# Performance work log

Measured on AMD Instinct MI355X. Metric: run time of the kernel, lower is better.

## Reference

```python
import jax, jax.numpy as jnp
import numpy as np

B, S, E, H, D = 4, 2048, 1024, 16, 64

def setup_inputs() -> dict:
    key = jax.random.key(0)
    ks = jax.random.split(key, 9)
    sc = 0.02
    return {
        "x":  jax.random.normal(ks[0], (B, S, E), jnp.float32),
        "Wq": jax.random.normal(ks[1], (H, E, D), jnp.float32) * sc,
        "bq": jax.random.normal(ks[2], (H, D), jnp.float32) * sc,
        "Wk": jax.random.normal(ks[3], (H, E, D), jnp.float32) * sc,
        "bk": jax.random.normal(ks[4], (H, D), jnp.float32) * sc,
        "Wv": jax.random.normal(ks[5], (H, E, D), jnp.float32) * sc,
        "bv": jax.random.normal(ks[6], (H, D), jnp.float32) * sc,
        "Wp": jax.random.normal(ks[7], (H * D, E), jnp.float32) * sc,
        "bp": jax.random.normal(ks[8], (E,), jnp.float32) * sc,
    }

def reference(x, Wq, bq, Wk, bk, Wv, bv, Wp, bp):
    # Per-head projections (stacked): [B,S,E] x [H,E,D] -> [B,H,S,D]
    q = jnp.einsum('bse,hed->bhsd', x, Wq) + bq[None, :, None, :]
    k = jnp.einsum('bse,hed->bhsd', x, Wk) + bk[None, :, None, :]
    v = jnp.einsum('bse,hed->bhsd', x, Wv) + bv[None, :, None, :]
    # Scaled scores with causal mask: [B,H,S,S]
    scores = jnp.einsum('bhqd,bhkd->bhqk', q, k) / jnp.sqrt(jnp.float32(D))
    causal = jnp.tril(jnp.ones((S, S), dtype=bool))
    scores = jnp.where(causal[None, None], scores, -jnp.inf)
    attn = jax.nn.softmax(scores, axis=-1)
    out = jnp.einsum('bhqk,bhkd->bhqd', attn, v)          # [B,H,S,D]
    out = out.transpose(0, 2, 1, 3).reshape(B, S, H * D)  # concat heads
    return out @ Wp + bp                                   # [B,S,E]
```

## Files before the change

kernel.cpp:

```cpp
#include <hip/hip_runtime.h>
#include <hip/hip_bf16.h>

#define B_ 4
#define S_ 2048
#define E_ 1024
#define H_ 16
#define D_ 64
#define QSCALE 0.18033688011112042f

typedef __attribute__((ext_vector_type(8))) short bf16x8;
typedef __attribute__((ext_vector_type(4))) float f32x4;
typedef __attribute__((ext_vector_type(16))) float f32x16;

__device__ __forceinline__ f32x4 mfma16(bf16x8 a, bf16x8 b, f32x4 c) {
    return __builtin_amdgcn_mfma_f32_16x16x32_bf16(a, b, c, 0, 0, 0);
}
__device__ __forceinline__ f32x16 mfma32(bf16x8 a, bf16x8 b, f32x16 c) {
    return __builtin_amdgcn_mfma_f32_32x32x16_bf16(a, b, c, 0, 0, 0);
}
__device__ __forceinline__ short f2bs(float f) {
    __hip_bfloat16 h = __float2bfloat16(f);
    return *reinterpret_cast<short*>(&h);
}

#define XSLAB 1032
#define WSLAB 1544

__global__ __launch_bounds__(256) void conv_wqkv(
    const float* __restrict__ Wq, const float* __restrict__ Wk,
    const float* __restrict__ Wv, short* __restrict__ WT)
{
    const int mat = blockIdx.x >> 4;
    const int kt  = blockIdx.x & 15;
    const int which = mat >> 4, h = mat & 15;
    const float* src = (which == 0 ? Wq : which == 1 ? Wk : Wv) + (size_t)h * E_ * D_;
    __shared__ float T[64][65];
    const int tid = threadIdx.x;
    const int k0 = kt * 64;
    #pragma unroll
    for (int it = 0; it < 4; ++it) {
        int lin = tid + it * 256;
        int kr = lin >> 4, dc = (lin & 15) * 4;
        const float4 v = *(const float4*)&src[(size_t)(k0 + kr) * D_ + dc];
        T[kr][dc] = v.x; T[kr][dc + 1] = v.y; T[kr][dc + 2] = v.z; T[kr][dc + 3] = v.w;
    }
    __syncthreads();
    #pragma unroll
    for (int it = 0; it < 4; ++it) {
        int lin = tid + it * 256;
        int dr = lin >> 4, kc = (lin & 15) * 4;
        ushort4 o;
        o.x = (unsigned short)f2bs(T[kc][dr]);
        o.y = (unsigned short)f2bs(T[kc + 1][dr]);
        o.z = (unsigned short)f2bs(T[kc + 2][dr]);
        o.w = (unsigned short)f2bs(T[kc + 3][dr]);
        *(ushort4*)&WT[((size_t)mat * 64 + dr) * E_ + k0 + kc] = o;
    }
}

__global__ __launch_bounds__(256) void conv_wp(
    const float* __restrict__ Wp, short* __restrict__ WpT)
{
    const int ktile = blockIdx.x & 15, ntile = blockIdx.x >> 4;
    const int k0 = ktile * 64, n0 = ntile * 64;
    __shared__ float T[64][65];
    const int tid = threadIdx.x;
    #pragma unroll
    for (int it = 0; it < 4; ++it) {
        int lin = tid + it * 256;
        int kr = lin >> 4, nc = (lin & 15) * 4;
        const float4 v = *(const float4*)&Wp[(size_t)(k0 + kr) * E_ + n0 + nc];
        T[kr][nc] = v.x; T[kr][nc + 1] = v.y; T[kr][nc + 2] = v.z; T[kr][nc + 3] = v.w;
    }
    __syncthreads();
    #pragma unroll
    for (int it = 0; it < 4; ++it) {
        int lin = tid + it * 256;
        int nr = lin >> 4, kc = (lin & 15) * 4;
        ushort4 o;
        o.x = (unsigned short)f2bs(T[kc][nr]);
        o.y = (unsigned short)f2bs(T[kc + 1][nr]);
        o.z = (unsigned short)f2bs(T[kc + 2][nr]);
        o.w = (unsigned short)f2bs(T[kc + 3][nr]);
        *(ushort4*)&WpT[(size_t)(n0 + nr) * E_ + k0 + kc] = o;
    }
}

__global__ __launch_bounds__(256, 2) void qkv_fused(
    const float* __restrict__ x, const short* __restrict__ WT,
    const float* __restrict__ bq, const float* __restrict__ bk,
    const float* __restrict__ bv,
    short* __restrict__ Qw, short* __restrict__ Kw, short* __restrict__ VTw)
{
    const int h = blockIdx.y;
    const int m0 = blockIdx.x * 128;
    __shared__ short SM[8 * XSLAB + 8 * WSLAB];
    short* Xs = SM;
    short* Ws = SM + 8 * XSLAB;

    const int tid = threadIdx.x;
    const int lane = tid & 63, w = tid >> 6;
    const int wm = w & 1, wn = w >> 1;
    const int l31 = lane & 31, hi = lane >> 5;
    const int cc = tid & 7, r8 = tid >> 3;

    f32x16 acc[2][3];
    #pragma unroll
    for (int mf = 0; mf < 2; ++mf)
        #pragma unroll
        for (int nf = 0; nf < 3; ++nf)
            #pragma unroll
            for (int i = 0; i < 16; ++i) acc[mf][nf][i] = 0.f;

    float4 xr[4][2];
    bf16x8 wr[6];

    #pragma unroll
    for (int it = 0; it < 4; ++it) {
        const float* p = &x[(size_t)(m0 + it * 32 + r8) * E_ + cc * 8];
        xr[it][0] = *(const float4*)p;
        xr[it][1] = *(const float4*)(p + 4);
    }
    #pragma unroll
    for (int it = 0; it < 6; ++it) {
        int rg = ((it >> 1) * 16 + h) * 64 + (it & 1) * 32 + r8;
        wr[it] = *(const bf16x8*)&WT[(size_t)rg * E_ + cc * 8];
    }

    for (int k0 = 0; k0 < E_; k0 += 64) {
        #pragma unroll
        for (int it = 0; it < 4; ++it) {
            bf16x8 pk;
            pk[0] = f2bs(xr[it][0].x); pk[1] = f2bs(xr[it][0].y);
            pk[2] = f2bs(xr[it][0].z); pk[3] = f2bs(xr[it][0].w);
            pk[4] = f2bs(xr[it][1].x); pk[5] = f2bs(xr[it][1].y);
            pk[6] = f2bs(xr[it][1].z); pk[7] = f2bs(xr[it][1].w);
            *(bf16x8*)&Xs[cc * XSLAB + (it * 32 + r8) * 8] = pk;
        }
        #pragma unroll
        for (int it = 0; it < 6; ++it)
            *(bf16x8*)&Ws[cc * WSLAB + (it * 32 + r8) * 8] = wr[it];
        __syncthreads();
        if (k0 + 64 < E_) {
            #pragma unroll
            for (int it = 0; it < 4; ++it) {
                const float* p = &x[(size_t)(m0 + it * 32 + r8) * E_ + k0 + 64 + cc * 8];
                xr[it][0] = *(const float4*)p;
                xr[it][1] = *(const float4*)(p + 4);
            }
            #pragma unroll
            for (int it = 0; it < 6; ++it) {
                int rg = ((it >> 1) * 16 + h) * 64 + (it & 1) * 32 + r8;
                wr[it] = *(const bf16x8*)&WT[(size_t)rg * E_ + k0 + 64 + cc * 8];
            }
        }
        #pragma unroll
        for (int ks = 0; ks < 4; ++ks) {
            const int ccr = ks * 2 + hi;
            bf16x8 a[2], b[3];
            #pragma unroll
            for (int mf = 0; mf < 2; ++mf)
                a[mf] = *(const bf16x8*)&Xs[ccr * XSLAB + (wm * 64 + mf * 32 + l31) * 8];
            #pragma unroll
            for (int nf = 0; nf < 3; ++nf)
                b[nf] = *(const bf16x8*)&Ws[ccr * WSLAB + (wn * 96 + nf * 32 + l31) * 8];
            #pragma unroll
            for (int mf = 0; mf < 2; ++mf)
                #pragma unroll
                for (int nf = 0; nf < 3; ++nf)
                    acc[mf][nf] = mfma32(a[mf], b[nf], acc[mf][nf]);
        }
        __syncthreads();
    }

    const int bb = m0 >> 11;
    const int s0 = m0 & (S_ - 1);
    const size_t qkbase = ((size_t)bb * H_ + h) * S_;
    short* Vr = SM;
    #pragma unroll
    for (int mf = 0; mf < 2; ++mf)
        #pragma unroll
        for (int nf = 0; nf < 3; ++nf) {
            const int ng = wn * 96 + nf * 32;
            const int mat = ng >> 6;
            const int d = (ng & 63) + l31;
            const int sl0 = wm * 64 + mf * 32 + 4 * hi;
            if (mat == 0) {
                const float bb_ = bq[h * D_ + d];
                #pragma unroll
                for (int rg = 0; rg < 16; ++rg) {
                    int s = s0 + sl0 + (rg & 3) + 8 * (rg >> 2);
                    Qw[(qkbase + s) * D_ + d] = f2bs((acc[mf][nf][rg] + bb_) * QSCALE);
                }
            } else if (mat == 1) {
                const float bb_ = bk[h * D_ + d];
                #pragma unroll
                for (int rg = 0; rg < 16; ++rg) {
                    int s = s0 + sl0 + (rg & 3) + 8 * (rg >> 2);
                    Kw[(qkbase + s) * D_ + d] = f2bs(acc[mf][nf][rg] + bb_);
                }
            } else {
                const float bb_ = bv[h * D_ + d];
                #pragma unroll
                for (int rg = 0; rg < 16; ++rg) {
                    int sl = sl0 + (rg & 3) + 8 * (rg >> 2);
                    Vr[d * 136 + sl] = f2bs(acc[mf][nf][rg] + bb_);
                }
            }
        }
    __syncthreads();
    const size_t vbase = ((size_t)bb * H_ + h) * (size_t)D_ * S_;
    const int sc = tid & 15, dr = tid >> 4;
    #pragma unroll
    for (int it = 0; it < 4; ++it) {
        int d = it * 16 + dr;
        *(bf16x8*)&VTw[vbase + (size_t)d * S_ + s0 + sc * 8] =
            *(const bf16x8*)&Vr[d * 136 + sc * 8];
    }
}

__global__ __launch_bounds__(256, 2) void attn(
    const short* __restrict__ Qw, const short* __restrict__ Kw,
    const short* __restrict__ VTw, short* __restrict__ Ow)
{
    const int jj = blockIdx.x;
    const int bh = blockIdx.y;
    const int b = bh >> 4, h = bh & 15;
    const size_t kbase = ((size_t)b * H_ + h) * (size_t)S_ * D_;
    const size_t vbase = ((size_t)b * H_ + h) * (size_t)D_ * S_;

    __shared__ short Qs[128 * 72];
    __shared__ short Ks[2][64 * 72];
    __shared__ short Vt[2][64 * 72];

    const int tid = threadIdx.x;
    const int lane = tid & 63, w = tid >> 6;
    const int l15 = lane & 15, qd = lane >> 4;

    const int r0s = tid >> 3;
    const int c0s = (tid & 7) * 8;
    const int r1s = r0s + 32;

    #pragma unroll
    for (int phase = 0; phase < 2; ++phase) {
        const int qt = phase ? jj : (15 - jj);

        #pragma unroll
        for (int it = 0; it < 4; ++it) {
            int row = w * 32 + it * 8 + (lane >> 3);
            int cb = (lane & 7) * 8;
            *(bf16x8*)&Qs[row * 72 + cb] =
                *(const bf16x8*)&Qw[kbase + (size_t)(qt * 128 + row) * D_ + cb];
        }
        asm volatile("s_waitcnt lgkmcnt(0)" ::: "memory");
        bf16x8 qf[2][2];
        #pragma unroll
        for (int mi = 0; mi < 2; ++mi)
            #pragma unroll
            for (int t = 0; t < 2; ++t)
                qf[mi][t] = *(const bf16x8*)&Qs[(w * 32 + mi * 16 + l15) * 72 + t * 32 + qd * 8];

        f32x4 zero = {0.f, 0.f, 0.f, 0.f};
        f32x4 oacc[2][4];
        float lrow[2][4];
        #pragma unroll
        for (int mi = 0; mi < 2; ++mi) {
            #pragma unroll
            for (int c = 0; c < 4; ++c) oacc[mi][c] = zero;
            #pragma unroll
            for (int r = 0; r < 4; ++r) lrow[mi][r] = 0.f;
        }

        const int nkt = (qt + 1) * 2;
        bf16x8 kr0, kr1, vr0, vr1;
        kr0 = *(const bf16x8*)&Kw[kbase + (size_t)r0s * D_ + c0s];
        kr1 = *(const bf16x8*)&Kw[kbase + (size_t)r1s * D_ + c0s];
        vr0 = *(const bf16x8*)&VTw[vbase + (size_t)r0s * S_ + c0s];
        vr1 = *(const bf16x8*)&VTw[vbase + (size_t)r1s * S_ + c0s];
        *(bf16x8*)&Ks[0][r0s * 72 + c0s] = kr0;
        *(bf16x8*)&Ks[0][r1s * 72 + c0s] = kr1;
        *(bf16x8*)&Vt[0][r0s * 72 + c0s] = vr0;
        *(bf16x8*)&Vt[0][r1s * 72 + c0s] = vr1;
        __syncthreads();

        int p = 0;
        for (int kt = 0; kt < nkt; ++kt) {
            const bool pre = (kt + 1 < nkt);
            if (pre) {
                kr0 = *(const bf16x8*)&Kw[kbase + (size_t)((kt + 1) * 64 + r0s) * D_ + c0s];
                kr1 = *(const bf16x8*)&Kw[kbase + (size_t)((kt + 1) * 64 + r1s) * D_ + c0s];
                vr0 = *(const bf16x8*)&VTw[vbase + (size_t)r0s * S_ + (kt + 1) * 64 + c0s];
                vr1 = *(const bf16x8*)&VTw[vbase + (size_t)r1s * S_ + (kt + 1) * 64 + c0s];
            }
            f32x4 sc[2][4];
            #pragma unroll
            for (int mi = 0; mi < 2; ++mi)
                #pragma unroll
                for (int c = 0; c < 4; ++c) sc[mi][c] = zero;
            #pragma unroll
            for (int t = 0; t < 2; ++t)
                #pragma unroll
                for (int c = 0; c < 4; ++c) {
                    bf16x8 bk = *(const bf16x8*)&Ks[p][(c * 16 + l15) * 72 + t * 32 + qd * 8];
                    sc[0][c] = mfma16(qf[0][t], bk, sc[0][c]);
                    sc[1][c] = mfma16(qf[1][t], bk, sc[1][c]);
                }
            #pragma unroll
            for (int mi = 0; mi < 2; ++mi) {
                const int fr = qt * 128 + w * 32 + mi * 16;
                if (kt * 64 + 63 > fr) {
                    #pragma unroll
                    for (int c = 0; c < 4; ++c) {
                        int col = kt * 64 + c * 16 + l15;
                        #pragma unroll
                        for (int r = 0; r < 4; ++r)
                            if (col > fr + qd * 4 + r) sc[mi][c][r] = -1e30f;
                    }
                }
                #pragma unroll
                for (int c = 0; c < 4; ++c)
                    #pragma unroll
                    for (int r = 0; r < 4; ++r) {
                        float pv = __builtin_amdgcn_exp2f(sc[mi][c][r]);
                        lrow[mi][r] += pv;
                        Qs[(w * 32 + mi * 16 + qd * 4 + r) * 72 + c * 16 + l15] = f2bs(pv);
                    }
            }
            asm volatile("s_waitcnt lgkmcnt(0)" ::: "memory");
            #pragma unroll
            for (int t = 0; t < 2; ++t) {
                bf16x8 ap0 = *(const bf16x8*)&Qs[(w * 32 + l15) * 72 + t * 32 + qd * 8];
                bf16x8 ap1 = *(const bf16x8*)&Qs[(w * 32 + 16 + l15) * 72 + t * 32 + qd * 8];
                #pragma unroll
                for (int c = 0; c < 4; ++c) {
                    bf16x8 bv = *(const bf16x8*)&Vt[p][(c * 16 + l15) * 72 + t * 32 + qd * 8];
                    oacc[0][c] = mfma16(ap0, bv, oacc[0][c]);
                    oacc[1][c] = mfma16(ap1, bv, oacc[1][c]);
                }
            }
            if (pre) {
                *(bf16x8*)&Ks[1 - p][r0s * 72 + c0s] = kr0;
                *(bf16x8*)&Ks[1 - p][r1s * 72 + c0s] = kr1;
                *(bf16x8*)&Vt[1 - p][r0s * 72 + c0s] = vr0;
                *(bf16x8*)&Vt[1 - p][r1s * 72 + c0s] = vr1;
            }
            __syncthreads();
            p ^= 1;
        }

        #pragma unroll
        for (int mi = 0; mi < 2; ++mi) {
            float inv[4];
            #pragma unroll
            for (int r = 0; r < 4; ++r) {
                float l = lrow[mi][r];
                l += __shfl_xor(l, 1);
                l += __shfl_xor(l, 2);
                l += __shfl_xor(l, 4);
                l += __shfl_xor(l, 8);
                inv[r] = 1.f / l;
            }
            #pragma unroll
            for (int c = 0; c < 4; ++c)
                #pragma unroll
                for (int r = 0; r < 4; ++r) {
                    int s = qt * 128 + w * 32 + mi * 16 + qd * 4 + r;
                    Ow[((size_t)b * S_ + s) * (H_ * D_) + h * D_ + c * 16 + l15] =
                        f2bs(oacc[mi][c][r] * inv[r]);
                }
        }
    }
}

__global__ __launch_bounds__(256, 2) void out_proj(
    const short* __restrict__ Oin, const short* __restrict__ WpT,
    const float* __restrict__ bp, float* __restrict__ out)
{
    const int m0 = blockIdx.x * 128;
    const int n0 = blockIdx.y * 128;
    __shared__ short SM2[16 * XSLAB];
    short* As = SM2;
    short* Bs = SM2 + 8 * XSLAB;

    const int tid = threadIdx.x;
    const int lane = tid & 63, w = tid >> 6;
    const int wm = w & 1, wn = w >> 1;
    const int l31 = lane & 31, hi = lane >> 5;
    const int cc = tid & 7, r8 = tid >> 3;

    f32x16 acc[2][2];
    #pragma unroll
    for (int mf = 0; mf < 2; ++mf)
        #pragma unroll
        for (int nf = 0; nf < 2; ++nf)
            #pragma unroll
            for (int i = 0; i < 16; ++i) acc[mf][nf][i] = 0.f;

    bf16x8 ar[4], br[4];
    #pragma unroll
    for (int it = 0; it < 4; ++it) {
        ar[it] = *(const bf16x8*)&Oin[(size_t)(m0 + it * 32 + r8) * E_ + cc * 8];
        br[it] = *(const bf16x8*)&WpT[(size_t)(n0 + it * 32 + r8) * E_ + cc * 8];
    }

    for (int k0 = 0; k0 < E_; k0 += 64) {
        #pragma unroll
        for (int it = 0; it < 4; ++it) {
            *(bf16x8*)&As[cc * XSLAB + (it * 32 + r8) * 8] = ar[it];
            *(bf16x8*)&Bs[cc * XSLAB + (it * 32 + r8) * 8] = br[it];
        }
        __syncthreads();
        if (k0 + 64 < E_) {
            #pragma unroll
            for (int it = 0; it < 4; ++it) {
                ar[it] = *(const bf16x8*)&Oin[(size_t)(m0 + it * 32 + r8) * E_ + k0 + 64 + cc * 8];
                br[it] = *(const bf16x8*)&WpT[(size_t)(n0 + it * 32 + r8) * E_ + k0 + 64 + cc * 8];
            }
        }
        #pragma unroll
        for (int ks = 0; ks < 4; ++ks) {
            const int ccr = ks * 2 + hi;
            bf16x8 a[2], b[2];
            #pragma unroll
            for (int mf = 0; mf < 2; ++mf)
                a[mf] = *(const bf16x8*)&As[ccr * XSLAB + (wm * 64 + mf * 32 + l31) * 8];
            #pragma unroll
            for (int nf = 0; nf < 2; ++nf)
                b[nf] = *(const bf16x8*)&Bs[ccr * XSLAB + (wn * 64 + nf * 32 + l31) * 8];
            #pragma unroll
            for (int mf = 0; mf < 2; ++mf)
                #pragma unroll
                for (int nf = 0; nf < 2; ++nf)
                    acc[mf][nf] = mfma32(a[mf], b[nf], acc[mf][nf]);
        }
        __syncthreads();
    }
    #pragma unroll
    for (int mf = 0; mf < 2; ++mf)
        #pragma unroll
        for (int nf = 0; nf < 2; ++nf) {
            const int n = n0 + wn * 64 + nf * 32 + l31;
            const float bpv = bp[n];
            const int sl0 = wm * 64 + mf * 32 + 4 * hi;
            #pragma unroll
            for (int rg = 0; rg < 16; ++rg) {
                int m = m0 + sl0 + (rg & 3) + 8 * (rg >> 2);
                out[(size_t)m * E_ + n] = acc[mf][nf][rg] + bpv;
            }
        }
}

extern "C" void kernel_launch(void* const* d_in, const int* in_sizes, int n_in,
                              void* d_out, int out_size, void* d_ws, size_t ws_size,
                              hipStream_t stream)
{
    const float* x  = (const float*)d_in[0];
    const float* Wq = (const float*)d_in[1];
    const float* bq = (const float*)d_in[2];
    const float* Wk = (const float*)d_in[3];
    const float* bk = (const float*)d_in[4];
    const float* Wv = (const float*)d_in[5];
    const float* bv = (const float*)d_in[6];
    const float* Wp = (const float*)d_in[7];
    const float* bp = (const float*)d_in[8];
    float* out = (float*)d_out;

    const size_t nQKV = (size_t)B_ * H_ * S_ * D_;
    short* Qw   = (short*)d_ws;
    short* Kw   = Qw + nQKV;
    short* VTw  = Kw + nQKV;
    short* buf3 = VTw + nQKV;
    short* WT   = buf3;
    short* Ow   = buf3;
    short* WpT  = Qw;

    conv_wqkv<<<dim3(768), 256, 0, stream>>>(Wq, Wk, Wv, WT);
    qkv_fused<<<dim3(64, 16), 256, 0, stream>>>(x, WT, bq, bk, bv, Qw, Kw, VTw);
    attn<<<dim3(8, 64), 256, 0, stream>>>(Qw, Kw, VTw, Ow);
    conv_wp<<<dim3(256), 256, 0, stream>>>(Wp, WpT);
    out_proj<<<dim3(64, 8), 256, 0, stream>>>(Ow, WpT, bp, out);
}
```

Before: 245.7 us.

## Pre-convert x to bf16 and stage GEMM tiles via direct global-to-LDS loads

x is now converted to bf16 once, inside the extra blocks of the weight-conversion kernel. Because of this, the QKV projection no longer converts fp32 rows 16 times, once per head. Both the QKV and output-projection GEMMs now fill shared memory with global_load_lds, which bypasses registers. The register-prefetch double buffering is dropped, and the slab padding is removed. Occupancy hints rise to 3 and 4 blocks per CU. In exchange, global-load latency is no longer overlapped with the previous tile's compute. The unpadded LDS layout may also cause bank conflicts.

```diff
diff --git a/kernel.cpp b/kernel.cpp
--- a/kernel.cpp
+++ b/kernel.cpp
@@ -23,19 +23,43 @@
     return *reinterpret_cast<short*>(&h);
 }
 
-#define XSLAB 1032
-#define WSLAB 1544
+__device__ __forceinline__ void gl16(const void* g, void* l) {
+    __builtin_amdgcn_global_load_lds(
+        (const __attribute__((address_space(1))) void*)g,
+        (__attribute__((address_space(3))) void*)l, 16, 0, 0);
+}
+
+#define XSLAB 1024
+#define WSLAB 1536
+#define PSLAB 1024
 
 __global__ __launch_bounds__(256) void conv_wqkv(
     const float* __restrict__ Wq, const float* __restrict__ Wk,
-    const float* __restrict__ Wv, short* __restrict__ WT)
-{
+    const float* __restrict__ Wv, short* __restrict__ WT,
+    const float* __restrict__ x, short* __restrict__ xb)
+{
+    __shared__ float T[64][65];
+    const int tid = threadIdx.x;
+    if (blockIdx.x >= 768) {
+        const int c = blockIdx.x - 768;
+        const float* xs = x + (size_t)c * 8192;
+        short* xd = xb + (size_t)c * 8192;
+        #pragma unroll
+        for (int it = 0; it < 4; ++it) {
+            const int off = it * 2048 + tid * 8;
+            const float4 a = *(const float4*)&xs[off];
+            const float4 b = *(const float4*)&xs[off + 4];
+            bf16x8 pk;
+            pk[0] = f2bs(a.x); pk[1] = f2bs(a.y); pk[2] = f2bs(a.z); pk[3] = f2bs(a.w);
+            pk[4] = f2bs(b.x); pk[5] = f2bs(b.y); pk[6] = f2bs(b.z); pk[7] = f2bs(b.w);
+            *(bf16x8*)&xd[off] = pk;
+        }
+        return;
+    }
     const int mat = blockIdx.x >> 4;
     const int kt  = blockIdx.x & 15;
     const int which = mat >> 4, h = mat & 15;
     const float* src = (which == 0 ? Wq : which == 1 ? Wk : Wv) + (size_t)h * E_ * D_;
-    __shared__ float T[64][65];
-    const int tid = threadIdx.x;
     const int k0 = kt * 64;
     #pragma unroll
     for (int it = 0; it < 4; ++it) {
@@ -86,8 +110,8 @@
     }
 }
 
-__global__ __launch_bounds__(256, 2) void qkv_fused(
-    const float* __restrict__ x, const short* __restrict__ WT,
+__global__ __launch_bounds__(256, 3) void qkv_fused(
+    const short* __restrict__ xb, const short* __restrict__ WT,
     const float* __restrict__ bq, const float* __restrict__ bk,
     const float* __restrict__ bv,
     short* __restrict__ Qw, short* __restrict__ Kw, short* __restrict__ VTw)
@@ -102,7 +126,6 @@
     const int lane = tid & 63, w = tid >> 6;
     const int wm = w & 1, wn = w >> 1;
     const int l31 = lane & 31, hi = lane >> 5;
-    const int cc = tid & 7, r8 = tid >> 3;
 
     f32x16 acc[2][3];
     #pragma unroll
@@ -112,48 +135,34 @@
             #pragma unroll
             for (int i = 0; i < 16; ++i) acc[mf][nf][i] = 0.f;
 
-    float4 xr[4][2];
-    bf16x8 wr[6];
-
-    #pragma unroll
-    for (int it = 0; it < 4; ++it) {
-        const float* p = &x[(size_t)(m0 + it * 32 + r8) * E_ + cc * 8];
-        xr[it][0] = *(const float4*)p;
-        xr[it][1] = *(const float4*)(p + 4);
-    }
-    #pragma unroll
-    for (int it = 0; it < 6; ++it) {
-        int rg = ((it >> 1) * 16 + h) * 64 + (it & 1) * 32 + r8;
-        wr[it] = *(const bf16x8*)&WT[(size_t)rg * E_ + cc * 8];
-    }
-
     for (int k0 = 0; k0 < E_; k0 += 64) {
         #pragma unroll
         for (int it = 0; it < 4; ++it) {
-            bf16x8 pk;
-            pk[0] = f2bs(xr[it][0].x); pk[1] = f2bs(xr[it][0].y);
-            pk[2] = f2bs(xr[it][0].z); pk[3] = f2bs(xr[it][0].w);
-            pk[4] = f2bs(xr[it][1].x); pk[5] = f2bs(xr[it][1].y);
-            pk[6] = f2bs(xr[it][1].z); pk[7] = f2bs(xr[it][1].w);
-            *(bf16x8*)&Xs[cc * XSLAB + (it * 32 + r8) * 8] = pk;
-        }
-        #pragma unroll
-        for (int it = 0; it < 6; ++it)
-            *(bf16x8*)&Ws[cc * WSLAB + (it * 32 + r8) * 8] = wr[it];
+            const int u = it * 256 + tid;
+            const int s = u >> 7, r = u & 127;
+            const int ub = it * 256 + (tid & 192);
+            gl16(&xb[(size_t)(m0 + r) * E_ + k0 + s * 8],
+                 &Xs[(ub >> 7) * XSLAB + (ub & 127) * 8]);
+        }
+        #pragma unroll
+        for (int it = 0; it < 4; ++it) {
+            const int u = it * 256 + tid;
+            const int s = u >> 7, r = u & 127;
+            const int ub = it * 256 + (tid & 192);
+            const int rg = ((r >> 6) * 16 + h) * 64 + (r & 63);
+            gl16(&WT[(size_t)rg * E_ + k0 + s * 8],
+                 &Ws[(ub >> 7) * WSLAB + (ub & 127) * 8]);
+        }
+        #pragma unroll
+        for (int it = 0; it < 2; ++it) {
+            const int u = it * 256 + tid;
+            const int s = u >> 6;
+            const int ub = it * 256 + (tid & 192);
+            const int rg = (32 + h) * 64 + (u & 63);
+            gl16(&WT[(size_t)rg * E_ + k0 + s * 8],
+                 &Ws[(ub >> 6) * WSLAB + 1024]);
+        }
         __syncthreads();
-        if (k0 + 64 < E_) {
-            #pragma unroll
-            for (int it = 0; it < 4; ++it) {
-                const float* p = &x[(size_t)(m0 + it * 32 + r8) * E_ + k0 + 64 + cc * 8];
-                xr[it][0] = *(const float4*)p;
-                xr[it][1] = *(const float4*)(p + 4);
-            }
-            #pragma unroll
-            for (int it = 0; it < 6; ++it) {
-                int rg = ((it >> 1) * 16 + h) * 64 + (it & 1) * 32 + r8;
-                wr[it] = *(const bf16x8*)&WT[(size_t)rg * E_ + k0 + 64 + cc * 8];
-            }
-        }
         #pragma unroll
         for (int ks = 0; ks < 4; ++ks) {
             const int ccr = ks * 2 + hi;
@@ -372,21 +381,20 @@
     }
 }
 
-__global__ __launch_bounds__(256, 2) void out_proj(
+__global__ __launch_bounds__(256, 4) void out_proj(
     const short* __restrict__ Oin, const short* __restrict__ WpT,
     const float* __restrict__ bp, float* __restrict__ out)
 {
     const int m0 = blockIdx.x * 128;
     const int n0 = blockIdx.y * 128;
-    __shared__ short SM2[16 * XSLAB];
+    __shared__ short SM2[16 * PSLAB];
     short* As = SM2;
-    short* Bs = SM2 + 8 * XSLAB;
+    short* Bs = SM2 + 8 * PSLAB;
 
     const int tid = threadIdx.x;
     const int lane = tid & 63, w = tid >> 6;
     const int wm = w & 1, wn = w >> 1;
     const int l31 = lane & 31, hi = lane >> 5;
-    const int cc = tid & 7, r8 = tid >> 3;
 
     f32x16 acc[2][2];
     #pragma unroll
@@ -396,37 +404,27 @@
             #pragma unroll
             for (int i = 0; i < 16; ++i) acc[mf][nf][i] = 0.f;
 
-    bf16x8 ar[4], br[4];
-    #pragma unroll
-    for (int it = 0; it < 4; ++it) {
-        ar[it] = *(const bf16x8*)&Oin[(size_t)(m0 + it * 32 + r8) * E_ + cc * 8];
-        br[it] = *(const bf16x8*)&WpT[(size_t)(n0 + it * 32 + r8) * E_ + cc * 8];
-    }
-
     for (int k0 = 0; k0 < E_; k0 += 64) {
         #pragma unroll
         for (int it = 0; it < 4; ++it) {
-            *(bf16x8*)&As[cc * XSLAB + (it * 32 + r8) * 8] = ar[it];
-            *(bf16x8*)&Bs[cc * XSLAB + (it * 32 + r8) * 8] = br[it];
+            const int u = it * 256 + tid;
+            const int s = u >> 7, r = u & 127;
+            const int ub = it * 256 + (tid & 192);
+            const int lo = (ub >> 7) * PSLAB + (ub & 127) * 8;
+            gl16(&Oin[(size_t)(m0 + r) * E_ + k0 + s * 8], &As[lo]);
+            gl16(&WpT[(size_t)(n0 + r) * E_ + k0 + s * 8], &Bs[lo]);
         }
         __syncthreads();
-        if (k0 + 64 < E_) {
-            #pragma unroll
-            for (int it = 0; it < 4; ++it) {
-                ar[it] = *(const bf16x8*)&Oin[(size_t)(m0 + it * 32 + r8) * E_ + k0 + 64 + cc * 8];
-                br[it] = *(const bf16x8*)&WpT[(size_t)(n0 + it * 32 + r8) * E_ + k0 + 64 + cc * 8];
-            }
-        }
         #pragma unroll
         for (int ks = 0; ks < 4; ++ks) {
             const int ccr = ks * 2 + hi;
             bf16x8 a[2], b[2];
             #pragma unroll
             for (int mf = 0; mf < 2; ++mf)
-                a[mf] = *(const bf16x8*)&As[ccr * XSLAB + (wm * 64 + mf * 32 + l31) * 8];
+                a[mf] = *(const bf16x8*)&As[ccr * PSLAB + (wm * 64 + mf * 32 + l31) * 8];
             #pragma unroll
             for (int nf = 0; nf < 2; ++nf)
-                b[nf] = *(const bf16x8*)&Bs[ccr * XSLAB + (wn * 64 + nf * 32 + l31) * 8];
+                b[nf] = *(const bf16x8*)&Bs[ccr * PSLAB + (wn * 64 + nf * 32 + l31) * 8];
             #pragma unroll
             for (int mf = 0; mf < 2; ++mf)
                 #pragma unroll
@@ -469,13 +467,13 @@
     short* Qw   = (short*)d_ws;
     short* Kw   = Qw + nQKV;
     short* VTw  = Kw + nQKV;
-    short* buf3 = VTw + nQKV;
-    short* WT   = buf3;
-    short* Ow   = buf3;
+    short* WT   = VTw + nQKV;
+    short* xb   = WT + (size_t)48 * 64 * E_;
+    short* Ow   = xb;
     short* WpT  = Qw;
 
-    conv_wqkv<<<dim3(768), 256, 0, stream>>>(Wq, Wk, Wv, WT);
-    qkv_fused<<<dim3(64, 16), 256, 0, stream>>>(x, WT, bq, bk, bv, Qw, Kw, VTw);
+    conv_wqkv<<<dim3(1792), 256, 0, stream>>>(Wq, Wk, Wv, WT, x, xb);
+    qkv_fused<<<dim3(64, 16), 256, 0, stream>>>(xb, WT, bq, bk, bv, Qw, Kw, VTw);
     attn<<<dim3(8, 64), 256, 0, stream>>>(Qw, Kw, VTw, Ow);
     conv_wp<<<dim3(256), 256, 0, stream>>>(Wp, WpT);
     out_proj<<<dim3(64, 8), 256, 0, stream>>>(Ow, WpT, bp, out);
```

Result: slower. 295.8 us (+20.4%).

## Pre-convert x to bf16 once and merge all conversion kernels into one launch

Applied to the files above, without the earlier changes.

A single conv_all kernel now converts the QKV weights, converts Wp, and casts x to bf16 in a dedicated workspace buffer. The QKV projection reads bf16 x, so each of the 16 head blocks per row tile no longer re-reads fp32 x and re-converts it. This halves the repeated global traffic for x and drops one kernel launch. The cost is an extra pass writing 16 MB of bf16 x and a larger workspace, since WpT, xb and Ow are now laid out separately.

```diff
diff --git a/kernel.cpp b/kernel.cpp
--- a/kernel.cpp
+++ b/kernel.cpp
@@ -26,45 +26,61 @@
 #define XSLAB 1032
 #define WSLAB 1544
 
-__global__ __launch_bounds__(256) void conv_wqkv(
+__global__ __launch_bounds__(256) void conv_all(
     const float* __restrict__ Wq, const float* __restrict__ Wk,
-    const float* __restrict__ Wv, short* __restrict__ WT)
+    const float* __restrict__ Wv, short* __restrict__ WT,
+    const float* __restrict__ x, short* __restrict__ xb,
+    const float* __restrict__ Wp, short* __restrict__ WpT)
 {
-    const int mat = blockIdx.x >> 4;
-    const int kt  = blockIdx.x & 15;
-    const int which = mat >> 4, h = mat & 15;
-    const float* src = (which == 0 ? Wq : which == 1 ? Wk : Wv) + (size_t)h * E_ * D_;
     __shared__ float T[64][65];
     const int tid = threadIdx.x;
-    const int k0 = kt * 64;
-    #pragma unroll
-    for (int it = 0; it < 4; ++it) {
-        int lin = tid + it * 256;
-        int kr = lin >> 4, dc = (lin & 15) * 4;
-        const float4 v = *(const float4*)&src[(size_t)(k0 + kr) * D_ + dc];
-        T[kr][dc] = v.x; T[kr][dc + 1] = v.y; T[kr][dc + 2] = v.z; T[kr][dc + 3] = v.w;
-    }
-    __syncthreads();
-    #pragma unroll
-    for (int it = 0; it < 4; ++it) {
-        int lin = tid + it * 256;
-        int dr = lin >> 4, kc = (lin & 15) * 4;
-        ushort4 o;
-        o.x = (unsigned short)f2bs(T[kc][dr]);
-        o.y = (unsigned short)f2bs(T[kc + 1][dr]);
-        o.z = (unsigned short)f2bs(T[kc + 2][dr]);
-        o.w = (unsigned short)f2bs(T[kc + 3][dr]);
-        *(ushort4*)&WT[((size_t)mat * 64 + dr) * E_ + k0 + kc] = o;
-    }
-}
-
-__global__ __launch_bounds__(256) void conv_wp(
-    const float* __restrict__ Wp, short* __restrict__ WpT)
-{
-    const int ktile = blockIdx.x & 15, ntile = blockIdx.x >> 4;
+    const int bid = blockIdx.x;
+    if (bid >= 768 && bid < 1792) {
+        const int c = bid - 768;
+        const float* xs = x + (size_t)c * 8192;
+        short* xd = xb + (size_t)c * 8192;
+        #pragma unroll
+        for (int it = 0; it < 4; ++it) {
+            const int off = it * 2048 + tid * 8;
+            const float4 a = *(const float4*)&xs[off];
+            const float4 b = *(const float4*)&xs[off + 4];
+            bf16x8 pk;
+            pk[0] = f2bs(a.x); pk[1] = f2bs(a.y); pk[2] = f2bs(a.z); pk[3] = f2bs(a.w);
+            pk[4] = f2bs(b.x); pk[5] = f2bs(b.y); pk[6] = f2bs(b.z); pk[7] = f2bs(b.w);
+            *(bf16x8*)&xd[off] = pk;
+        }
+        return;
+    }
+    if (bid < 768) {
+        const int mat = bid >> 4;
+        const int kt  = bid & 15;
+        const int which = mat >> 4, h = mat & 15;
+        const float* src = (which == 0 ? Wq : which == 1 ? Wk : Wv) + (size_t)h * E_ * D_;
+        const int k0 = kt * 64;
+        #pragma unroll
+        for (int it = 0; it < 4; ++it) {
+            int lin = tid + it * 256;
+            int kr = lin >> 4, dc = (lin & 15) * 4;
+            const float4 v = *(const float4*)&src[(size_t)(k0 + kr) * D_ + dc];
+            T[kr][dc] = v.x; T[kr][dc + 1] = v.y; T[kr][dc + 2] = v.z; T[kr][dc + 3] = v.w;
+        }
+        __syncthreads();
+        #pragma unroll
+        for (int it = 0; it < 4; ++it) {
+            int lin = tid + it * 256;
+            int dr = lin >> 4, kc = (lin & 15) * 4;
+            ushort4 o;
+            o.x = (unsigned short)f2bs(T[kc][dr]);
+            o.y = (unsigned short)f2bs(T[kc + 1][dr]);
+            o.z = (unsigned short)f2bs(T[kc + 2][dr]);
+            o.w = (unsigned short)f2bs(T[kc + 3][dr]);
+            *(ushort4*)&WT[((size_t)mat * 64 + dr) * E_ + k0 + kc] = o;
+        }
+        return;
+    }
+    const int idx = bid - 1792;
+    const int ktile = idx & 15, ntile = idx >> 4;
     const int k0 = ktile * 64, n0 = ntile * 64;
-    __shared__ float T[64][65];
-    const int tid = threadIdx.x;
     #pragma unroll
     for (int it = 0; it < 4; ++it) {
         int lin = tid + it * 256;
@@ -87,7 +103,7 @@
 }
 
 __global__ __launch_bounds__(256, 2) void qkv_fused(
-    const float* __restrict__ x, const short* __restrict__ WT,
+    const short* __restrict__ xb, const short* __restrict__ WT,
     const float* __restrict__ bq, const float* __restrict__ bk,
     const float* __restrict__ bv,
     short* __restrict__ Qw, short* __restrict__ Kw, short* __restrict__ VTw)
@@ -112,15 +128,12 @@
             #pragma unroll
             for (int i = 0; i < 16; ++i) acc[mf][nf][i] = 0.f;
 
-    float4 xr[4][2];
+    bf16x8 xr[4];
     bf16x8 wr[6];
 
     #pragma unroll
-    for (int it = 0; it < 4; ++it) {
-        const float* p = &x[(size_t)(m0 + it * 32 + r8) * E_ + cc * 8];
-        xr[it][0] = *(const float4*)p;
-        xr[it][1] = *(const float4*)(p + 4);
-    }
+    for (int it = 0; it < 4; ++it)
+        xr[it] = *(const bf16x8*)&xb[(size_t)(m0 + it * 32 + r8) * E_ + cc * 8];
     #pragma unroll
     for (int it = 0; it < 6; ++it) {
         int rg = ((it >> 1) * 16 + h) * 64 + (it & 1) * 32 + r8;
@@ -129,25 +142,16 @@
 
     for (int k0 = 0; k0 < E_; k0 += 64) {
         #pragma unroll
-        for (int it = 0; it < 4; ++it) {
-            bf16x8 pk;
-            pk[0] = f2bs(xr[it][0].x); pk[1] = f2bs(xr[it][0].y);
-            pk[2] = f2bs(xr[it][0].z); pk[3] = f2bs(xr[it][0].w);
-            pk[4] = f2bs(xr[it][1].x); pk[5] = f2bs(xr[it][1].y);
-            pk[6] = f2bs(xr[it][1].z); pk[7] = f2bs(xr[it][1].w);
-            *(bf16x8*)&Xs[cc * XSLAB + (it * 32 + r8) * 8] = pk;
-        }
+        for (int it = 0; it < 4; ++it)
+            *(bf16x8*)&Xs[cc * XSLAB + (it * 32 + r8) * 8] = xr[it];
         #pragma unroll
         for (int it = 0; it < 6; ++it)
             *(bf16x8*)&Ws[cc * WSLAB + (it * 32 + r8) * 8] = wr[it];
         __syncthreads();
         if (k0 + 64 < E_) {
             #pragma unroll
-            for (int it = 0; it < 4; ++it) {
-                const float* p = &x[(size_t)(m0 + it * 32 + r8) * E_ + k0 + 64 + cc * 8];
-                xr[it][0] = *(const float4*)p;
-                xr[it][1] = *(const float4*)(p + 4);
-            }
+            for (int it = 0; it < 4; ++it)
+                xr[it] = *(const bf16x8*)&xb[(size_t)(m0 + it * 32 + r8) * E_ + k0 + 64 + cc * 8];
             #pragma unroll
             for (int it = 0; it < 6; ++it) {
                 int rg = ((it >> 1) * 16 + h) * 64 + (it & 1) * 32 + r8;
@@ -469,14 +473,13 @@
     short* Qw   = (short*)d_ws;
     short* Kw   = Qw + nQKV;
     short* VTw  = Kw + nQKV;
-    short* buf3 = VTw + nQKV;
-    short* WT   = buf3;
-    short* Ow   = buf3;
-    short* WpT  = Qw;
-
-    conv_wqkv<<<dim3(768), 256, 0, stream>>>(Wq, Wk, Wv, WT);
-    qkv_fused<<<dim3(64, 16), 256, 0, stream>>>(x, WT, bq, bk, bv, Qw, Kw, VTw);
+    short* WT   = VTw + nQKV;
+    short* xb   = WT + (size_t)48 * 64 * E_;
+    short* WpT  = xb + (size_t)8192 * E_;
+    short* Ow   = xb;
+
+    conv_all<<<dim3(2048), 256, 0, stream>>>(Wq, Wk, Wv, WT, x, xb, Wp, WpT);
+    qkv_fused<<<dim3(64, 16), 256, 0, stream>>>(xb, WT, bq, bk, bv, Qw, Kw, VTw);
     attn<<<dim3(8, 64), 256, 0, stream>>>(Qw, Kw, VTw, Ow);
-    conv_wp<<<dim3(256), 256, 0, stream>>>(Wp, WpT);
     out_proj<<<dim3(64, 8), 256, 0, stream>>>(Ow, WpT, bp, out);
 }
```

After: 243.9 us. No clear change (-0.8%).
